# Kernel tuning notes

Measured on AMD Instinct MI355X. Metric: run time of the kernel, lower is better.

Reference implementation:

```python
import jax, jax.numpy as jnp
import numpy as np
import math

DIM = 1024
NUM_HEADS = 16
HEAD_DIM = DIM // NUM_HEADS
BLOCK_SIZE = 64


def _block_mask(src_blocks, tgt_blocks, num_blocks):
    # Block-level BigBird mask: global first/last block columns, sliding window of 1, random blocks.
    i = jnp.arange(num_blocks)[:, None]
    j = jnp.arange(num_blocks)[None, :]
    band = jnp.abs(i - j) <= 1
    glob = (j == 0) | (j == num_blocks - 1)
    bm = band | glob
    bm = bm.at[src_blocks, tgt_blocks].set(True)
    return bm  # [nb, nb] bool


def setup_inputs() -> dict:
    key = jax.random.key(0)
    ks = jax.random.split(key, 12)
    B, S = 2, 2048
    x = jax.random.normal(ks[0], (B, S, DIM), dtype=jnp.float32)
    scale = 0.02
    Wq = jax.random.normal(ks[1], (DIM, DIM), dtype=jnp.float32) * scale
    bq = jnp.zeros((DIM,), dtype=jnp.float32)
    Wk = jax.random.normal(ks[2], (DIM, DIM), dtype=jnp.float32) * scale
    bk = jnp.zeros((DIM,), dtype=jnp.float32)
    Wv = jax.random.normal(ks[3], (DIM, DIM), dtype=jnp.float32) * scale
    bv = jnp.zeros((DIM,), dtype=jnp.float32)
    Wo = jax.random.normal(ks[4], (DIM, DIM), dtype=jnp.float32) * scale
    bo = jnp.zeros((DIM,), dtype=jnp.float32)
    num_blocks = S // BLOCK_SIZE
    src_blocks = jax.random.randint(ks[5], (3,), 0, num_blocks, dtype=jnp.int32)
    tgt_blocks = jax.random.randint(ks[6], (3,), 0, num_blocks, dtype=jnp.int32)
    return {"x": x, "Wq": Wq, "bq": bq, "Wk": Wk, "bk": bk, "Wv": Wv, "bv": bv,
            "Wo": Wo, "bo": bo, "src_blocks": src_blocks, "tgt_blocks": tgt_blocks}


def reference(x, Wq, bq, Wk, bk, Wv, bv, Wo, bo, src_blocks, tgt_blocks):
    B, S, _ = x.shape
    nb = S // BLOCK_SIZE
    # NOTE: original torch code uses .view (not transpose) to split heads; replicate faithfully.
    q = (x @ Wq.T + bq).reshape(B, NUM_HEADS, S, HEAD_DIM)
    k = (x @ Wk.T + bk).reshape(B, NUM_HEADS, S, HEAD_DIM)
    v = (x @ Wv.T + bv).reshape(B, NUM_HEADS, S, HEAD_DIM)
    bm = _block_mask(src_blocks, tgt_blocks, nb)
    mask = jnp.repeat(jnp.repeat(bm, BLOCK_SIZE, axis=0), BLOCK_SIZE, axis=1)  # [S, S]
    scores = jnp.einsum('bhqd,bhkd->bhqk', q, k) / math.sqrt(HEAD_DIM)
    scores = jnp.where(mask[None, None], scores, jnp.float32(-1e9))
    attn = jax.nn.softmax(scores, axis=-1)
    out = jnp.einsum('bhqk,bhkd->bhqd', attn, v)
    out = out.transpose(0, 2, 1, 3).reshape(B, S, DIM)
    return out @ Wo.T + bo
```

## Files before the change

kernel.cpp:

```cpp
#include <hip/hip_runtime.h>
#include <math.h>

typedef __attribute__((ext_vector_type(8))) short short8;
typedef __attribute__((ext_vector_type(4))) float f32x4;

#define SEQ 2048
#define NB  32

__device__ __forceinline__ unsigned short f2bf(float f) {
    unsigned u = __float_as_uint(f);
    u = (u + 0x7FFFu + ((u >> 16) & 1u)) >> 16;
    return (unsigned short)u;
}

__global__ __launch_bounds__(256) void cvt_bf16(const float* __restrict__ in,
                                                unsigned short* __restrict__ out, int n8) {
    int i = blockIdx.x * 256 + threadIdx.x;
    const int stride = gridDim.x * 256;
    for (; i < n8; i += stride) {
        const float4 a = ((const float4*)in)[i * 2];
        const float4 b = ((const float4*)in)[i * 2 + 1];
        uint4 o;
        o.x = f2bf(a.x) | ((unsigned)f2bf(a.y) << 16);
        o.y = f2bf(a.z) | ((unsigned)f2bf(a.w) << 16);
        o.z = f2bf(b.x) | ((unsigned)f2bf(b.y) << 16);
        o.w = f2bf(b.z) | ((unsigned)f2bf(b.w) << 16);
        ((uint4*)out)[i] = o;
    }
}

template <int BF16OUT>
__global__ __launch_bounds__(256) void gemm_bt(const unsigned short* __restrict__ A,
                                               const unsigned short* __restrict__ Wall,
                                               const float* __restrict__ b0,
                                               const float* __restrict__ b1,
                                               const float* __restrict__ b2,
                                               unsigned short* __restrict__ outb,
                                               float* __restrict__ outf) {
    __shared__ __align__(16) unsigned short As[128 * 32];
    __shared__ __align__(16) unsigned short Bs[128 * 32];

    const int t = threadIdx.x;
    const int w = t >> 6, l = t & 63;
    const int which = blockIdx.x >> 3;
    const int n0 = (blockIdx.x & 7) * 128;
    const int m0 = blockIdx.y * 128;
    const unsigned short* W = Wall + (size_t)which * (1024ull * 1024);
    const float* bias = (which == 0) ? b0 : (which == 1) ? b1 : b2;

    const int wr = (w >> 1) * 64, wc = (w & 1) * 64;
    f32x4 acc[4][4];
#pragma unroll
    for (int i = 0; i < 4; ++i)
#pragma unroll
        for (int j = 0; j < 4; ++j) acc[i][j] = f32x4{0.f, 0.f, 0.f, 0.f};

    const int srow = t >> 2;
    const int skk = (t & 3) * 8;

    uint4 a0 = *(const uint4*)&A[(size_t)(m0 + srow) * 1024 + skk];
    uint4 a1 = *(const uint4*)&A[(size_t)(m0 + 64 + srow) * 1024 + skk];
    uint4 w0 = *(const uint4*)&W[(size_t)(n0 + srow) * 1024 + skk];
    uint4 w1 = *(const uint4*)&W[(size_t)(n0 + 64 + srow) * 1024 + skk];

    for (int kt = 0; kt < 32; ++kt) {
        __syncthreads();
        *(uint4*)&As[srow * 32 + skk] = a0;
        *(uint4*)&As[(64 + srow) * 32 + skk] = a1;
        *(uint4*)&Bs[srow * 32 + skk] = w0;
        *(uint4*)&Bs[(64 + srow) * 32 + skk] = w1;
        __syncthreads();

        if (kt + 1 < 32) {
            const int k0 = (kt + 1) * 32;
            a0 = *(const uint4*)&A[(size_t)(m0 + srow) * 1024 + k0 + skk];
            a1 = *(const uint4*)&A[(size_t)(m0 + 64 + srow) * 1024 + k0 + skk];
            w0 = *(const uint4*)&W[(size_t)(n0 + srow) * 1024 + k0 + skk];
            w1 = *(const uint4*)&W[(size_t)(n0 + 64 + srow) * 1024 + k0 + skk];
        }

        short8 af[4], bf[4];
#pragma unroll
        for (int mi = 0; mi < 4; ++mi)
            af[mi] = *(const short8*)&As[(wr + mi * 16 + (l & 15)) * 32 + (l >> 4) * 8];
#pragma unroll
        for (int ni = 0; ni < 4; ++ni)
            bf[ni] = *(const short8*)&Bs[(wc + ni * 16 + (l & 15)) * 32 + (l >> 4) * 8];
#pragma unroll
        for (int mi = 0; mi < 4; ++mi)
#pragma unroll
            for (int ni = 0; ni < 4; ++ni)
                acc[mi][ni] = __builtin_amdgcn_mfma_f32_16x16x32_bf16(af[mi], bf[ni],
                                                                      acc[mi][ni], 0, 0, 0);
    }

    const int g = l >> 4, c = l & 15;
#pragma unroll
    for (int ni = 0; ni < 4; ++ni) {
        const int n = n0 + wc + ni * 16 + c;
        const float bv = bias[n];
#pragma unroll
        for (int mi = 0; mi < 4; ++mi) {
#pragma unroll
            for (int j = 0; j < 4; ++j) {
                const size_t m = (size_t)(m0 + wr + mi * 16 + g * 4 + j);
                const float v = acc[mi][ni][j] + bv;
                if (BF16OUT)
                    (outb + (size_t)which * (4096ull * 1024))[m * 1024 + n] = f2bf(v);
                else
                    outf[m * 1024 + n] = v;
            }
        }
    }
}

__global__ __launch_bounds__(256) void transpose_v(const unsigned short* __restrict__ v,
                                                   unsigned short* __restrict__ vt) {
    __shared__ __align__(16) unsigned short L[64][72];
    const int t = threadIdx.x;
    const int st = blockIdx.x;
    const int ht = blockIdx.y;
    const int b = blockIdx.z;
    {
        const int r = t >> 2, cs = t & 3;
        const unsigned short* src =
            v + (size_t)(b * 16 + ht) * (SEQ * 64) + (size_t)(st * 64 + r) * 64 + cs * 16;
        *(uint4*)&L[r][cs * 16] = *(const uint4*)src;
        *(uint4*)&L[r][cs * 16 + 8] = *(const uint4*)(src + 8);
    }
    __syncthreads();
    {
        const int dr = t >> 2, ss = t & 3;
        unsigned short tmp[16];
#pragma unroll
        for (int e = 0; e < 16; ++e) tmp[e] = L[ss * 16 + e][dr];
        unsigned short* dst =
            vt + (size_t)(b * 16 + ht) * (SEQ * 64) + (size_t)dr * SEQ + st * 64 + ss * 16;
        *(uint4*)dst = *(uint4*)&tmp[0];
        *(uint4*)(dst + 8) = *(uint4*)&tmp[8];
    }
}

__global__ __launch_bounds__(256) void attn_mfma(const unsigned short* __restrict__ qb_,
                                                 const unsigned short* __restrict__ kb_,
                                                 const unsigned short* __restrict__ vtb_,
                                                 const int* __restrict__ srcb,
                                                 const int* __restrict__ tgtb,
                                                 unsigned short* __restrict__ outb) {
    __shared__ __align__(16) unsigned short Ks[64 * 72];
    __shared__ __align__(16) unsigned short Vs[64 * 72];
    __shared__ __align__(16) unsigned short Ps[4][16 * 72];

    const int t = threadIdx.x, w = t >> 6, l = t & 63;
    const int qi = blockIdx.x, h = blockIdx.y, b = blockIdx.z;
    const int g = l >> 4, c = l & 15;

    unsigned mask = 1u | (1u << (NB - 1)) | (1u << qi);
    if (qi > 0) mask |= 1u << (qi - 1);
    if (qi < NB - 1) mask |= 1u << (qi + 1);
#pragma unroll
    for (int tt = 0; tt < 3; ++tt)
        if (srcb[tt] == qi) mask |= 1u << (tgtb[tt] & 31);

    const size_t ho = (size_t)(b * 16 + h) * (SEQ * 64);
    const unsigned short* Q = qb_ + ho;
    const unsigned short* K = kb_ + ho;
    const unsigned short* VT = vtb_ + ho;

    short8 qf[2];
    {
        const unsigned short* qrow = Q + (size_t)(qi * 64 + w * 16 + c) * 64;
        qf[0] = *(const short8*)(qrow + g * 8);
        qf[1] = *(const short8*)(qrow + 32 + g * 8);
    }

    f32x4 oacc[4];
#pragma unroll
    for (int d = 0; d < 4; ++d) oacc[d] = f32x4{0.f, 0.f, 0.f, 0.f};
    float mrun = -INFINITY, lsum = 0.f;

    const int sr = t >> 2, sc = (t & 3) * 16;

    for (int kb = 0; kb < NB; ++kb) {
        if (!((mask >> kb) & 1u)) continue;

        const unsigned short* ksrc = K + (size_t)(kb * 64 + sr) * 64 + sc;
        const unsigned short* vsrc = VT + (size_t)sr * SEQ + kb * 64 + sc;
        uint4 k0 = *(const uint4*)ksrc, k1 = *(const uint4*)(ksrc + 8);
        uint4 v0 = *(const uint4*)vsrc, v1 = *(const uint4*)(vsrc + 8);

        __syncthreads();
        *(uint4*)&Ks[sr * 72 + sc] = k0;
        *(uint4*)&Ks[sr * 72 + sc + 8] = k1;
        *(uint4*)&Vs[sr * 72 + sc] = v0;
        *(uint4*)&Vs[sr * 72 + sc + 8] = v1;
        __syncthreads();

        f32x4 sacc[4];
#pragma unroll
        for (int kt = 0; kt < 4; ++kt) sacc[kt] = f32x4{0.f, 0.f, 0.f, 0.f};
#pragma unroll
        for (int kt = 0; kt < 4; ++kt) {
#pragma unroll
            for (int ks = 0; ks < 2; ++ks) {
                const short8 ka = *(const short8*)&Ks[(kt * 16 + c) * 72 + ks * 32 + g * 8];
                sacc[kt] = __builtin_amdgcn_mfma_f32_16x16x32_bf16(ka, qf[ks], sacc[kt], 0, 0, 0);
            }
        }

        float sv[16];
        float tmax = -INFINITY;
#pragma unroll
        for (int kt = 0; kt < 4; ++kt)
#pragma unroll
            for (int j = 0; j < 4; ++j) {
                const float x = sacc[kt][j] * 0.125f;
                sv[kt * 4 + j] = x;
                tmax = fmaxf(tmax, x);
            }
        tmax = fmaxf(tmax, __shfl_xor(tmax, 16));
        tmax = fmaxf(tmax, __shfl_xor(tmax, 32));
        const float newm = fmaxf(mrun, tmax);
        const float corr = __expf(mrun - newm);
        float ps = 0.f;
#pragma unroll
        for (int e = 0; e < 16; ++e) {
            const float p = __expf(sv[e] - newm);
            sv[e] = p;
            ps += p;
        }
        ps += __shfl_xor(ps, 16);
        ps += __shfl_xor(ps, 32);
        lsum = lsum * corr + ps;
        mrun = newm;
#pragma unroll
        for (int d = 0; d < 4; ++d)
#pragma unroll
            for (int j = 0; j < 4; ++j) oacc[d][j] *= corr;

        unsigned short* pw = &Ps[w][c * 72];
#pragma unroll
        for (int kt = 0; kt < 4; ++kt) {
            uint2 pk;
            pk.x = f2bf(sv[kt * 4 + 0]) | ((unsigned)f2bf(sv[kt * 4 + 1]) << 16);
            pk.y = f2bf(sv[kt * 4 + 2]) | ((unsigned)f2bf(sv[kt * 4 + 3]) << 16);
            *(uint2*)&pw[kt * 16 + g * 4] = pk;
        }
        asm volatile("s_waitcnt lgkmcnt(0)" ::: "memory");
        __builtin_amdgcn_sched_barrier(0);

#pragma unroll
        for (int ks = 0; ks < 2; ++ks) {
            const short8 pb = *(const short8*)&Ps[w][c * 72 + ks * 32 + g * 8];
#pragma unroll
            for (int dt = 0; dt < 4; ++dt) {
                const short8 va = *(const short8*)&Vs[(dt * 16 + c) * 72 + ks * 32 + g * 8];
                oacc[dt] = __builtin_amdgcn_mfma_f32_16x16x32_bf16(va, pb, oacc[dt], 0, 0, 0);
            }
        }
    }

    const float inv = 1.f / lsum;
    unsigned short* orow = outb + (size_t)(b * SEQ + qi * 64 + w * 16 + c) * 1024 + h * 64;
#pragma unroll
    for (int dt = 0; dt < 4; ++dt)
#pragma unroll
        for (int j = 0; j < 4; ++j)
            orow[dt * 16 + g * 4 + j] = f2bf(oacc[dt][j] * inv);
}

extern "C" void kernel_launch(void* const* d_in, const int* in_sizes, int n_in,
                              void* d_out, int out_size, void* d_ws, size_t ws_size,
                              hipStream_t stream) {
    const float* x  = (const float*)d_in[0];
    const float* Wq = (const float*)d_in[1];
    const float* bq = (const float*)d_in[2];
    const float* Wk = (const float*)d_in[3];
    const float* bk = (const float*)d_in[4];
    const float* Wv = (const float*)d_in[5];
    const float* bv = (const float*)d_in[6];
    const float* Wo = (const float*)d_in[7];
    const float* bo = (const float*)d_in[8];
    const int* srcb = (const int*)d_in[9];
    const int* tgtb = (const int*)d_in[10];

    unsigned short* wsu = (unsigned short*)d_ws;
    unsigned short* xbf   = wsu;
    unsigned short* wqkv  = wsu + 4194304ull;
    unsigned short* wobf  = wsu + 7340032ull;
    unsigned short* qkvbf = wsu + 8388608ull;
    unsigned short* vtbf  = wsu + 20971520ull;
    unsigned short* attbf = wsu + 25165824ull;

    hipLaunchKernelGGL(cvt_bf16, dim3(1024), dim3(256), 0, stream, x, xbf, 524288);
    hipLaunchKernelGGL(cvt_bf16, dim3(512), dim3(256), 0, stream, Wq, wqkv, 131072);
    hipLaunchKernelGGL(cvt_bf16, dim3(512), dim3(256), 0, stream, Wk, wqkv + 1048576ull, 131072);
    hipLaunchKernelGGL(cvt_bf16, dim3(512), dim3(256), 0, stream, Wv, wqkv + 2097152ull, 131072);
    hipLaunchKernelGGL(cvt_bf16, dim3(512), dim3(256), 0, stream, Wo, wobf, 131072);

    hipLaunchKernelGGL((gemm_bt<1>), dim3(24, 32), dim3(256), 0, stream,
                       xbf, wqkv, bq, bk, bv, qkvbf, (float*)nullptr);

    hipLaunchKernelGGL(transpose_v, dim3(32, 16, 2), dim3(256), 0, stream,
                       qkvbf + 2ull * 4194304ull, vtbf);

    hipLaunchKernelGGL(attn_mfma, dim3(32, 16, 2), dim3(256), 0, stream,
                       qkvbf, qkvbf + 4194304ull, vtbf, srcb, tgtb, attbf);

    hipLaunchKernelGGL((gemm_bt<0>), dim3(8, 32), dim3(256), 0, stream,
                       attbf, wobf, bo, bo, bo, (unsigned short*)nullptr, (float*)d_out);

    (void)in_sizes; (void)n_in; (void)out_size; (void)ws_size;
}
```

Before: 107.2 us.

## Use direct global-to-LDS loads in GEMM, merge weight casts, narrow output-projection tile

The GEMM now stages A and W tiles with global_load_lds, writing 16-byte chunks straight into shared memory and dropping the register round-trip. In exchange it loses the previous register prefetch of the next K tile, so loads are no longer overlapped with MFMA work. The four weight-conversion launches are merged into one kernel with a 4-row grid to cut launch overhead. The output projection uses a new 64-column tile variant, doubling its block count to fill more compute units.

```diff
diff --git a/kernel.cpp b/kernel.cpp
--- a/kernel.cpp
+++ b/kernel.cpp
@@ -11,6 +11,12 @@
     unsigned u = __float_as_uint(f);
     u = (u + 0x7FFFu + ((u >> 16) & 1u)) >> 16;
     return (unsigned short)u;
+}
+
+__device__ __forceinline__ void gload16(const unsigned short* g, unsigned short* l) {
+    __builtin_amdgcn_global_load_lds(
+        (__attribute__((address_space(1))) void*)(void*)(g),
+        (__attribute__((address_space(3))) void*)(l), 16, 0, 0);
 }
 
 __global__ __launch_bounds__(256) void cvt_bf16(const float* __restrict__ in,
@@ -29,7 +35,32 @@
     }
 }
 
-template <int BF16OUT>
+__global__ __launch_bounds__(256) void cvt_w4(const float* __restrict__ w0,
+                                              const float* __restrict__ w1,
+                                              const float* __restrict__ w2,
+                                              const float* __restrict__ w3,
+                                              unsigned short* __restrict__ o0,
+                                              unsigned short* __restrict__ o1,
+                                              unsigned short* __restrict__ o2,
+                                              unsigned short* __restrict__ o3) {
+    const int which = blockIdx.y;
+    const float* in = (which == 0) ? w0 : (which == 1) ? w1 : (which == 2) ? w2 : w3;
+    unsigned short* out = (which == 0) ? o0 : (which == 1) ? o1 : (which == 2) ? o2 : o3;
+    int i = blockIdx.x * 256 + threadIdx.x;
+    const int stride = gridDim.x * 256;
+    for (; i < 131072; i += stride) {
+        const float4 a = ((const float4*)in)[i * 2];
+        const float4 b = ((const float4*)in)[i * 2 + 1];
+        uint4 o;
+        o.x = f2bf(a.x) | ((unsigned)f2bf(a.y) << 16);
+        o.y = f2bf(a.z) | ((unsigned)f2bf(a.w) << 16);
+        o.z = f2bf(b.x) | ((unsigned)f2bf(b.y) << 16);
+        o.w = f2bf(b.z) | ((unsigned)f2bf(b.w) << 16);
+        ((uint4*)out)[i] = o;
+    }
+}
+
+template <int BF16OUT, int BN>
 __global__ __launch_bounds__(256) void gemm_bt(const unsigned short* __restrict__ A,
                                                const unsigned short* __restrict__ Wall,
                                                const float* __restrict__ b0,
@@ -37,70 +68,66 @@
                                                const float* __restrict__ b2,
                                                unsigned short* __restrict__ outb,
                                                float* __restrict__ outf) {
+    constexpr int MI = (BN == 128) ? 4 : 2;
+    constexpr int NI = 4;
     __shared__ __align__(16) unsigned short As[128 * 32];
-    __shared__ __align__(16) unsigned short Bs[128 * 32];
+    __shared__ __align__(16) unsigned short Bs[BN * 32];
 
     const int t = threadIdx.x;
     const int w = t >> 6, l = t & 63;
-    const int which = blockIdx.x >> 3;
-    const int n0 = (blockIdx.x & 7) * 128;
+    const int bx = blockIdx.x;
+    const int which = (BN == 128) ? (bx >> 3) : 0;
+    const int n0 = (BN == 128) ? (bx & 7) * 128 : bx * 64;
     const int m0 = blockIdx.y * 128;
     const unsigned short* W = Wall + (size_t)which * (1024ull * 1024);
     const float* bias = (which == 0) ? b0 : (which == 1) ? b1 : b2;
 
-    const int wr = (w >> 1) * 64, wc = (w & 1) * 64;
-    f32x4 acc[4][4];
-#pragma unroll
-    for (int i = 0; i < 4; ++i)
-#pragma unroll
-        for (int j = 0; j < 4; ++j) acc[i][j] = f32x4{0.f, 0.f, 0.f, 0.f};
-
-    const int srow = t >> 2;
-    const int skk = (t & 3) * 8;
-
-    uint4 a0 = *(const uint4*)&A[(size_t)(m0 + srow) * 1024 + skk];
-    uint4 a1 = *(const uint4*)&A[(size_t)(m0 + 64 + srow) * 1024 + skk];
-    uint4 w0 = *(const uint4*)&W[(size_t)(n0 + srow) * 1024 + skk];
-    uint4 w1 = *(const uint4*)&W[(size_t)(n0 + 64 + srow) * 1024 + skk];
+    const int wr = (BN == 128) ? (w >> 1) * 64 : w * 32;
+    const int wc = (BN == 128) ? (w & 1) * 64 : 0;
+
+    f32x4 acc[MI][NI];
+#pragma unroll
+    for (int i = 0; i < MI; ++i)
+#pragma unroll
+        for (int j = 0; j < NI; ++j) acc[i][j] = f32x4{0.f, 0.f, 0.f, 0.f};
+
+    const unsigned short* Ag = A + (size_t)(m0 + w * 32 + (l >> 2)) * 1024 + (l & 3) * 8;
+    const unsigned short* Wg =
+        W + (size_t)(n0 + ((BN == 128) ? w * 32 : w * 16) + (l >> 2)) * 1024 + (l & 3) * 8;
+    unsigned short* AsW = As + w * 1024;
+    unsigned short* BsW = Bs + ((BN == 128) ? w * 1024 : w * 512);
 
     for (int kt = 0; kt < 32; ++kt) {
+        const int k0 = kt * 32;
         __syncthreads();
-        *(uint4*)&As[srow * 32 + skk] = a0;
-        *(uint4*)&As[(64 + srow) * 32 + skk] = a1;
-        *(uint4*)&Bs[srow * 32 + skk] = w0;
-        *(uint4*)&Bs[(64 + srow) * 32 + skk] = w1;
+        gload16(Ag + k0, AsW);
+        gload16(Ag + k0 + 16 * 1024, AsW + 512);
+        gload16(Wg + k0, BsW);
+        if (BN == 128) gload16(Wg + k0 + 16 * 1024, BsW + 512);
         __syncthreads();
 
-        if (kt + 1 < 32) {
-            const int k0 = (kt + 1) * 32;
-            a0 = *(const uint4*)&A[(size_t)(m0 + srow) * 1024 + k0 + skk];
-            a1 = *(const uint4*)&A[(size_t)(m0 + 64 + srow) * 1024 + k0 + skk];
-            w0 = *(const uint4*)&W[(size_t)(n0 + srow) * 1024 + k0 + skk];
-            w1 = *(const uint4*)&W[(size_t)(n0 + 64 + srow) * 1024 + k0 + skk];
-        }
-
-        short8 af[4], bf[4];
-#pragma unroll
-        for (int mi = 0; mi < 4; ++mi)
+        short8 af[MI], bfr[NI];
+#pragma unroll
+        for (int mi = 0; mi < MI; ++mi)
             af[mi] = *(const short8*)&As[(wr + mi * 16 + (l & 15)) * 32 + (l >> 4) * 8];
 #pragma unroll
-        for (int ni = 0; ni < 4; ++ni)
-            bf[ni] = *(const short8*)&Bs[(wc + ni * 16 + (l & 15)) * 32 + (l >> 4) * 8];
-#pragma unroll
-        for (int mi = 0; mi < 4; ++mi)
-#pragma unroll
-            for (int ni = 0; ni < 4; ++ni)
-                acc[mi][ni] = __builtin_amdgcn_mfma_f32_16x16x32_bf16(af[mi], bf[ni],
+        for (int ni = 0; ni < NI; ++ni)
+            bfr[ni] = *(const short8*)&Bs[(wc + ni * 16 + (l & 15)) * 32 + (l >> 4) * 8];
+#pragma unroll
+        for (int mi = 0; mi < MI; ++mi)
+#pragma unroll
+            for (int ni = 0; ni < NI; ++ni)
+                acc[mi][ni] = __builtin_amdgcn_mfma_f32_16x16x32_bf16(af[mi], bfr[ni],
                                                                       acc[mi][ni], 0, 0, 0);
     }
 
     const int g = l >> 4, c = l & 15;
 #pragma unroll
-    for (int ni = 0; ni < 4; ++ni) {
+    for (int ni = 0; ni < NI; ++ni) {
         const int n = n0 + wc + ni * 16 + c;
         const float bv = bias[n];
 #pragma unroll
-        for (int mi = 0; mi < 4; ++mi) {
+        for (int mi = 0; mi < MI; ++mi) {
 #pragma unroll
             for (int j = 0; j < 4; ++j) {
                 const size_t m = (size_t)(m0 + wr + mi * 16 + g * 4 + j);
@@ -293,12 +320,11 @@
     unsigned short* attbf = wsu + 25165824ull;
 
     hipLaunchKernelGGL(cvt_bf16, dim3(1024), dim3(256), 0, stream, x, xbf, 524288);
-    hipLaunchKernelGGL(cvt_bf16, dim3(512), dim3(256), 0, stream, Wq, wqkv, 131072);
-    hipLaunchKernelGGL(cvt_bf16, dim3(512), dim3(256), 0, stream, Wk, wqkv + 1048576ull, 131072);
-    hipLaunchKernelGGL(cvt_bf16, dim3(512), dim3(256), 0, stream, Wv, wqkv + 2097152ull, 131072);
-    hipLaunchKernelGGL(cvt_bf16, dim3(512), dim3(256), 0, stream, Wo, wobf, 131072);
-
-    hipLaunchKernelGGL((gemm_bt<1>), dim3(24, 32), dim3(256), 0, stream,
+    hipLaunchKernelGGL(cvt_w4, dim3(512, 4), dim3(256), 0, stream,
+                       Wq, Wk, Wv, Wo,
+                       wqkv, wqkv + 1048576ull, wqkv + 2097152ull, wobf);
+
+    hipLaunchKernelGGL((gemm_bt<1, 128>), dim3(24, 32), dim3(256), 0, stream,
                        xbf, wqkv, bq, bk, bv, qkvbf, (float*)nullptr);
 
     hipLaunchKernelGGL(transpose_v, dim3(32, 16, 2), dim3(256), 0, stream,
@@ -307,7 +333,7 @@
     hipLaunchKernelGGL(attn_mfma, dim3(32, 16, 2), dim3(256), 0, stream,
                        qkvbf, qkvbf + 4194304ull, vtbf, srcb, tgtb, attbf);
 
-    hipLaunchKernelGGL((gemm_bt<0>), dim3(8, 32), dim3(256), 0, stream,
+    hipLaunchKernelGGL((gemm_bt<0, 64>), dim3(16, 32), dim3(256), 0, stream,
                        attbf, wobf, bo, bo, bo, (unsigned short*)nullptr, (float*)d_out);
 
     (void)in_sizes; (void)n_in; (void)out_size; (void)ws_size;
```

Result: faster. 97.53 us (-9.0%).
